# Optimization experiments

Hardware: AMD Instinct MI355X
Metric: run time of the kernel (lower is better)

## Reference

```python
import jax, jax.numpy as jnp
import numpy as np
import math

B, S, H = 2, 2048, 2048
NH, HD = 16, 128
THETA = 10000.0
NEG = -1e9


def make_rope_tables(seq_len, head_dim, theta):
    inv_freq = 1.0 / (theta ** (np.arange(0, head_dim, 2, dtype=np.float32) / head_dim))
    pos = np.arange(seq_len, dtype=np.float32)
    freqs = np.outer(pos, inv_freq)                    # (S, HD/2)
    emb = np.concatenate([freqs, freqs], axis=-1)      # (S, HD)
    return jnp.asarray(np.cos(emb)), jnp.asarray(np.sin(emb))


def setup_inputs() -> dict:
    key = jax.random.key(0)
    k1, k2, k3 = jax.random.split(key, 3)
    hidden_states = jax.random.normal(k1, (B, S, H), dtype=jnp.float32)
    rope_cos, rope_sin = make_rope_tables(S, HD, THETA)
    # additive causal mask [1,1,S,S]
    causal = jnp.tril(jnp.ones((S, S), dtype=bool))
    attention_mask = jnp.where(causal, 0.0, NEG).astype(jnp.float32)[None, None]
    w_qkv = jax.random.normal(k2, (3 * H, H), dtype=jnp.float32) * (1.0 / math.sqrt(H))
    w_o = jax.random.normal(k3, (H, H), dtype=jnp.float32) * (1.0 / math.sqrt(H))
    return {"hidden_states": hidden_states, "rope_cos": rope_cos, "rope_sin": rope_sin,
            "attention_mask": attention_mask, "w_qkv": w_qkv, "w_o": w_o}


def apply_rope(x, cos, sin):
    # x: (B, NH, S, HD); cos/sin: (S, HD)
    half = x.shape[-1] // 2
    x1, x2 = x[..., :half], x[..., half:]
    x_rot = jnp.concatenate([-x2, x1], axis=-1)
    return x * cos[None, None] + x_rot * sin[None, None]


def reference(hidden_states, rope_cos, rope_sin, attention_mask, w_qkv, w_o):
    b, s, h = hidden_states.shape
    qkv = hidden_states @ w_qkv.T                      # (B, S, 3H)
    qkv = qkv.reshape(b, s, 3, NH, HD).transpose(2, 0, 3, 1, 4)  # (3, B, NH, S, HD)
    q, k, v = qkv[0], qkv[1], qkv[2]
    q = apply_rope(q, rope_cos, rope_sin)
    k = apply_rope(k, rope_cos, rope_sin)
    scale = 1.0 / math.sqrt(HD)
    scores = jnp.einsum('bhqd,bhkd->bhqk', q, k) * scale + attention_mask
    probs = jax.nn.softmax(scores.astype(jnp.float32), axis=-1).astype(q.dtype)
    out = jnp.einsum('bhqk,bhkd->bhqd', probs, v)      # (B, NH, S, HD)
    out = out.transpose(0, 2, 1, 3).reshape(b, s, h)
    return out @ w_o.T
```

## Files before the change

kernel.cpp:

```cpp
#include <hip/hip_runtime.h>
#include <stdint.h>

typedef unsigned int u32;
typedef unsigned short u16;

typedef __bf16 bf16x8 __attribute__((ext_vector_type(8)));
typedef float f32x4 __attribute__((ext_vector_type(4)));

struct alignas(16) V16 { u32 a, b, c, d; };

__device__ __forceinline__ u16 f2bf(float x) {
    u32 u = __float_as_uint(x);
    u += 0x7FFFu + ((u >> 16) & 1u);
    return (u16)(u >> 16);
}
__device__ __forceinline__ float bf2f(u16 h) {
    return __uint_as_float(((u32)h) << 16);
}

__device__ __forceinline__ bf16x8 ld_frag(const u16* p) {
    return __builtin_bit_cast(bf16x8, *(const V16*)p);
}

__device__ __forceinline__ void async_cp16(u16* lds_dst, const u16* g_src) {
    __builtin_amdgcn_global_load_lds(
        (__attribute__((address_space(1))) void*)g_src,
        (__attribute__((address_space(3))) void*)lds_dst, 16, 0, 0);
}

__global__ __launch_bounds__(256) void cast_all_kernel(
    const float* __restrict__ hidden, const float* __restrict__ wqkv,
    const float* __restrict__ wo,
    u16* __restrict__ hA, u16* __restrict__ wqb, u16* __restrict__ wob)
{
    int i = blockIdx.x * 256 + threadIdx.x;
    const float* src; u16* dst; int off;
    if (i < 2097152)      { src = hidden; dst = hA;  off = i; }
    else if (i < 5242880) { src = wqkv;   dst = wqb; off = i - 2097152; }
    else                  { src = wo;     dst = wob; off = i - 5242880; }
    const float* p = src + (size_t)off * 4;
    ushort4 o;
    o.x = f2bf(p[0]); o.y = f2bf(p[1]); o.z = f2bf(p[2]); o.w = f2bf(p[3]);
    *(ushort4*)(dst + (size_t)off * 4) = o;
}

__device__ __forceinline__ void stage_half(
    u16* smem, const u16* __restrict__ Ag, const u16* __restrict__ Bg,
    int K, int isB, int kk, int buf, int th, int w, int rg0, int chl)
{
    const u16* G = isB ? Bg : Ag;
    u16* base = smem + isB * 32768 + buf * 16384 + kk * 8192;
    const int kcol = th * 64 + kk * 32;
#pragma unroll
    for (int i = 0; i < 2; ++i) {
        const int s = i * 8 + w;
        const int rg = s * 16 + rg0;
        async_cp16(base + s * 512, G + (size_t)rg * K + kcol + chl * 8);
    }
}

__global__ __launch_bounds__(512, 2) void gemm256(
    const u16* __restrict__ A, const u16* __restrict__ Bt,
    int M, int N, int K, int mode,
    float* __restrict__ Cout,
    u16* __restrict__ Qb, u16* __restrict__ Kb, u16* __restrict__ Vtb)
{
    extern __shared__ u16 smem[];
    const int t = threadIdx.x;
    const int w = t >> 6, l = t & 63;
    const int lr = l & 15, lk = (l >> 4) * 8;
    const int wm16 = (w >> 2) * 8;
    const int wn16 = (w & 3) * 4;
    const int laneoff = lr * 32 + (lk ^ ((lr & 8) ? 16 : 0));
    const int rg0 = l >> 2;
    const int chl = (l & 3) ^ ((l >> 4) & 2);

    const int flat = blockIdx.y * gridDim.x + blockIdx.x;
    const int xcd = flat & 7, slot = flat >> 3;
    const int cpx = gridDim.x >> 3;
    const int ncol = xcd * cpx + slot % cpx;
    const int mrow = slot / cpx;
    const int m0 = mrow * 256, n0 = ncol * 256;

    const u16* Ag = A + (size_t)m0 * K;
    const u16* Bg = Bt + (size_t)n0 * K;

    f32x4 acc[8][4];
#pragma unroll
    for (int i = 0; i < 8; ++i)
#pragma unroll
        for (int j = 0; j < 4; ++j) acc[i][j] = f32x4{0.f, 0.f, 0.f, 0.f};

    const int NT = K >> 6;

    stage_half(smem, Ag, Bg, K, 0, 0, 0, 0, w, rg0, chl);
    stage_half(smem, Ag, Bg, K, 1, 0, 0, 0, w, rg0, chl);
    stage_half(smem, Ag, Bg, K, 0, 1, 0, 0, w, rg0, chl);
    stage_half(smem, Ag, Bg, K, 1, 1, 0, 0, w, rg0, chl);
    stage_half(smem, Ag, Bg, K, 0, 0, 1, 1, w, rg0, chl);
    stage_half(smem, Ag, Bg, K, 1, 0, 1, 1, w, rg0, chl);
    asm volatile("s_waitcnt vmcnt(8)" ::: "memory");
    __builtin_amdgcn_s_barrier();

    for (int tt = 0; tt < NT; tt += 2) {
#pragma unroll
        for (int sub = 0; sub < 2; ++sub) {
            const int tcur = tt + sub;
            const u16* Abuf = smem + sub * 16384;
            const u16* Bbuf = smem + 32768 + sub * 16384;
            bf16x8 bfr[4];
#pragma unroll
            for (int p = 0; p < 4; ++p) {
                const int kk = p >> 1, mh = p & 1;
                const u16* Ab = Abuf + kk * 8192;
                const u16* Bb = Bbuf + kk * 8192;
                if (mh == 0) {
#pragma unroll
                    for (int ni = 0; ni < 4; ++ni)
                        bfr[ni] = ld_frag(Bb + (wn16 + ni) * 512 + laneoff);
                }
                bf16x8 af[4];
#pragma unroll
                for (int i = 0; i < 4; ++i)
                    af[i] = ld_frag(Ab + (wm16 + mh * 4 + i) * 512 + laneoff);

                if (p == 0 && tcur + 1 < NT)
                    stage_half(smem, Ag, Bg, K, 0, 1, sub ^ 1, tcur + 1, w, rg0, chl);
                if (p == 1 && tcur + 1 < NT)
                    stage_half(smem, Ag, Bg, K, 1, 1, sub ^ 1, tcur + 1, w, rg0, chl);
                if (p == 2 && tcur + 2 < NT)
                    stage_half(smem, Ag, Bg, K, 0, 0, sub, tcur + 2, w, rg0, chl);
                if (p == 3 && tcur + 2 < NT)
                    stage_half(smem, Ag, Bg, K, 1, 0, sub, tcur + 2, w, rg0, chl);

                if (p == 1) {
                    if (tcur < NT - 1) asm volatile("s_waitcnt vmcnt(8)" ::: "memory");
                    else               asm volatile("s_waitcnt vmcnt(0)" ::: "memory");
                }
                if (p == 3) {
                    if (tcur < NT - 2)       asm volatile("s_waitcnt vmcnt(8)" ::: "memory");
                    else if (tcur == NT - 2) asm volatile("s_waitcnt vmcnt(4)" ::: "memory");
                }
                __builtin_amdgcn_s_barrier();
                __builtin_amdgcn_s_setprio(1);
#pragma unroll
                for (int i = 0; i < 4; ++i)
#pragma unroll
                    for (int ni = 0; ni < 4; ++ni)
                        acc[mh * 4 + i][ni] = __builtin_amdgcn_mfma_f32_16x16x32_bf16(
                            af[i], bfr[ni], acc[mh * 4 + i][ni], 0, 0, 0);
                __builtin_amdgcn_s_setprio(0);
                __builtin_amdgcn_s_barrier();
            }
        }
    }

    __syncthreads();
    const int lrow4 = (l >> 4) * 4;
    const int wm0 = (w >> 2) * 128, wn0 = (w & 3) * 64;

    if (mode == 1) {
#pragma unroll
        for (int mi = 0; mi < 8; ++mi)
#pragma unroll
            for (int ni = 0; ni < 4; ++ni)
#pragma unroll
                for (int r = 0; r < 4; ++r) {
                    int gr = m0 + wm0 + mi * 16 + lrow4 + r;
                    int gc = n0 + wn0 + ni * 16 + lr;
                    Cout[(size_t)gr * N + gc] = acc[mi][ni][r];
                }
        return;
    }

    const int which = n0 >> 11;
    const int nh0 = (n0 & 2047) >> 7;
    const int bb = m0 >> 11;
    const int s0 = m0 & 2047;

    if (which < 2) {
#pragma unroll
        for (int mi = 0; mi < 8; ++mi)
#pragma unroll
            for (int ni = 0; ni < 4; ++ni)
#pragma unroll
                for (int r = 0; r < 4; ++r)
                    smem[(wm0 + mi * 16 + lrow4 + r) * 256 + wn0 + ni * 16 + lr] =
                        f2bf(acc[mi][ni][r]);
    } else {
#pragma unroll
        for (int mi = 0; mi < 8; ++mi)
#pragma unroll
            for (int ni = 0; ni < 4; ++ni)
#pragma unroll
                for (int r = 0; r < 4; ++r) {
                    int cr = wn0 + ni * 16 + lr;
                    int cc = wm0 + mi * 16 + lrow4 + r;
                    smem[cr * 256 + (cc ^ ((cr & 7) << 3))] = f2bf(acc[mi][ni][r]);
                }
    }
    __syncthreads();

    if (which < 2) {
        u16* dstb = (which == 0 ? Qb : Kb);
#pragma unroll
        for (int ps = 0; ps < 16; ++ps) {
            int chunk = ps * 512 + t;
            int row = chunk >> 5;
            int ce = (chunk & 31) * 8;
            int head = nh0 + (ce >> 7);
            int d = ce & 127;
            *(V16*)&dstb[((size_t)(bb * 16 + head) * 2048 + s0 + row) * 128 + d] =
                *(const V16*)&smem[row * 256 + ce];
        }
    } else {
#pragma unroll
        for (int ps = 0; ps < 16; ++ps) {
            int chunk = ps * 512 + t;
            int drow = chunk >> 5;
            int se = (chunk & 31) * 8;
            int head = nh0 + (drow >> 7);
            int d = drow & 127;
            *(V16*)&Vtb[((size_t)(bb * 16 + head) * 128 + d) * 2048 + s0 + se] =
                *(const V16*)&smem[drow * 256 + (se ^ ((drow & 7) << 3))];
        }
    }
}

__global__ __launch_bounds__(256) void rope_kernel(
    u16* __restrict__ Qb, u16* __restrict__ Kb,
    const float* __restrict__ cosT, const float* __restrict__ sinT, float qscale)
{
    int idx = blockIdx.x * 256 + threadIdx.x;
    int d = (idx & 7) * 8;
    int s = (idx >> 3) & 2047;
    int bh = idx >> 14;
    size_t base = ((size_t)bh * 2048 + s) * 128;
    float c[8], sn[8];
#pragma unroll
    for (int i = 0; i < 8; ++i) {
        c[i]  = cosT[s * 128 + d + i];
        sn[i] = sinT[s * 128 + d + i];
    }
    union U { V16 v; u16 h[8]; };
    U qlo, qhi, klo, khi, a, bq, ak, bk;
    qlo.v = *(const V16*)&Qb[base + d];
    qhi.v = *(const V16*)&Qb[base + d + 64];
    klo.v = *(const V16*)&Kb[base + d];
    khi.v = *(const V16*)&Kb[base + d + 64];
#pragma unroll
    for (int i = 0; i < 8; ++i) {
        float q1 = bf2f(qlo.h[i]), q2 = bf2f(qhi.h[i]);
        a.h[i]  = f2bf((q1 * c[i] - q2 * sn[i]) * qscale);
        bq.h[i] = f2bf((q2 * c[i] + q1 * sn[i]) * qscale);
        float k1 = bf2f(klo.h[i]), k2 = bf2f(khi.h[i]);
        ak.h[i] = f2bf(k1 * c[i] - k2 * sn[i]);
        bk.h[i] = f2bf(k2 * c[i] + k1 * sn[i]);
    }
    *(V16*)&Qb[base + d]      = a.v;
    *(V16*)&Qb[base + d + 64] = bq.v;
    *(V16*)&Kb[base + d]      = ak.v;
    *(V16*)&Kb[base + d + 64] = bk.v;
}

#define PS_LD 72
__global__ __launch_bounds__(256, 2) void flash_attn(
    const u16* __restrict__ Qb, const u16* __restrict__ Kb, const u16* __restrict__ Vtb,
    u16* __restrict__ ctx)
{
    __shared__ u16 Ks[2 * 64 * 128];
    __shared__ u16 Vts[2 * 128 * 64];
    __shared__ u16 Ps[4 * 16 * PS_LD];

    const int t = threadIdx.x, w = t >> 6, l = t & 63;
    const int lr = l & 15, lk = (l >> 4) * 8, lrow4 = (l >> 4) * 4;
    const int hi = l >> 4;
    const int xw = lr & 7;
    const int bh = blockIdx.x;
    const int pidx = blockIdx.y;
    const int wm = w * 16;

    const u16* Qg = Qb + (size_t)bh * 2048 * 128;
    const u16* Kg = Kb + (size_t)bh * 2048 * 128;
    const u16* Vg = Vtb + (size_t)bh * 128 * 2048;
    u16* Pw = &Ps[w * 16 * PS_LD];

    const int krow_l = l >> 4;
    const int vrow_l = l >> 3;
    const int vchk = ((l & 7) ^ vrow_l) * 8;

    const int b = bh >> 4, nh = bh & 15;

#pragma unroll
    for (int half = 0; half < 2; ++half) {
        const int qt = half ? pidx : 31 - pidx;
        const int q0 = qt * 64;

        bf16x8 qfrag[4];
#pragma unroll
        for (int kc = 0; kc < 4; ++kc)
            qfrag[kc] = ld_frag(&Qg[(size_t)(q0 + wm + lr) * 128 + kc * 32 + lk]);

        f32x4 oacc[8];
#pragma unroll
        for (int jo = 0; jo < 8; ++jo) oacc[jo] = f32x4{0.f, 0.f, 0.f, 0.f};
        float l_part[4] = {0.f, 0.f, 0.f, 0.f};

        const int ktiles = qt + 1;

#pragma unroll
        for (int it = 0; it < 4; ++it) {
            const int krow = it * 4 + krow_l;
            const int kchk = ((l & 15) ^ (krow & 7)) * 8;
            async_cp16(&Ks[w * 2048 + it * 512],
                       Kg + (size_t)(w * 16 + krow) * 128 + kchk);
        }
#pragma unroll
        for (int it = 0; it < 4; ++it) {
            const int vrow = w * 32 + it * 8 + vrow_l;
            async_cp16(&Vts[w * 2048 + it * 512],
                       Vg + (size_t)vrow * 2048 + vchk);
        }

        for (int kt = 0; kt < ktiles; ++kt) {
            const int buf = kt & 1;
            if (kt + 1 < ktiles) {
                const int c0n = (kt + 1) * 64;
                const int bo = (buf ^ 1) * 8192;
#pragma unroll
                for (int it = 0; it < 4; ++it) {
                    const int krow = it * 4 + krow_l;
                    const int kchk = ((l & 15) ^ (krow & 7)) * 8;
                    async_cp16(&Ks[bo + w * 2048 + it * 512],
                               Kg + (size_t)(c0n + w * 16 + krow) * 128 + kchk);
                }
#pragma unroll
                for (int it = 0; it < 4; ++it) {
                    const int vrow = w * 32 + it * 8 + vrow_l;
                    async_cp16(&Vts[bo + w * 2048 + it * 512],
                               Vg + (size_t)vrow * 2048 + c0n + vchk);
                }
                asm volatile("s_waitcnt vmcnt(8)" ::: "memory");
            } else {
                asm volatile("s_waitcnt vmcnt(0)" ::: "memory");
            }
            __builtin_amdgcn_s_barrier();

            const u16* Ksb = Ks + buf * 8192;
            const u16* Vsb = Vts + buf * 8192;

            f32x4 pacc[4];
#pragma unroll
            for (int j = 0; j < 4; ++j) pacc[j] = f32x4{0.f, 0.f, 0.f, 0.f};
#pragma unroll
            for (int kc = 0; kc < 4; ++kc) {
                const int kco = ((kc * 4 + hi) ^ xw) * 8;
                bf16x8 bk[4];
#pragma unroll
                for (int j = 0; j < 4; ++j)
                    bk[j] = ld_frag(&Ksb[(j * 16 + lr) * 128 + kco]);
#pragma unroll
                for (int j = 0; j < 4; ++j)
                    pacc[j] = __builtin_amdgcn_mfma_f32_16x16x32_bf16(qfrag[kc], bk[j], pacc[j], 0, 0, 0);
            }

            if (kt == qt) {
#pragma unroll
                for (int j = 0; j < 4; ++j) {
                    const int cl = j * 16 + lr;
#pragma unroll
                    for (int r = 0; r < 4; ++r) {
                        float pv = (cl > wm + lrow4 + r) ? 0.f : __expf(pacc[j][r]);
                        pacc[j][r] = pv;
                        l_part[r] += pv;
                    }
                }
            } else {
#pragma unroll
                for (int j = 0; j < 4; ++j)
#pragma unroll
                    for (int r = 0; r < 4; ++r) {
                        float pv = __expf(pacc[j][r]);
                        pacc[j][r] = pv;
                        l_part[r] += pv;
                    }
            }

#pragma unroll
            for (int j = 0; j < 4; ++j)
#pragma unroll
                for (int r = 0; r < 4; ++r)
                    Pw[(lrow4 + r) * PS_LD + j * 16 + lr] = f2bf(pacc[j][r]);

#pragma unroll
            for (int kc = 0; kc < 2; ++kc) {
                bf16x8 ap = ld_frag(&Pw[lr * PS_LD + kc * 32 + lk]);
                const int vco = ((kc * 4 + hi) ^ xw) * 8;
#pragma unroll
                for (int jo = 0; jo < 8; ++jo) {
                    bf16x8 bv = ld_frag(&Vsb[(jo * 16 + lr) * 64 + vco]);
                    oacc[jo] = __builtin_amdgcn_mfma_f32_16x16x32_bf16(ap, bv, oacc[jo], 0, 0, 0);
                }
            }
            __builtin_amdgcn_s_barrier();
        }

        float linv[4];
#pragma unroll
        for (int r = 0; r < 4; ++r) {
            float s = l_part[r];
#pragma unroll
            for (int dd = 8; dd >= 1; dd >>= 1) s += __shfl_xor(s, dd);
            linv[r] = __builtin_amdgcn_rcpf(s);
        }
#pragma unroll
        for (int jo = 0; jo < 8; ++jo)
#pragma unroll
            for (int r = 0; r < 4; ++r) {
                int srow2 = q0 + wm + lrow4 + r;
                int col = nh * 128 + jo * 16 + lr;
                ctx[((size_t)b * 2048 + srow2) * 2048 + col] = f2bf(oacc[jo][r] * linv[r]);
            }
    }
}

extern "C" void kernel_launch(void* const* d_in, const int* in_sizes, int n_in,
                              void* d_out, int out_size, void* d_ws, size_t ws_size,
                              hipStream_t stream)
{
    (void)in_sizes; (void)n_in; (void)out_size; (void)ws_size;
    const float* hidden = (const float*)d_in[0];
    const float* cosT   = (const float*)d_in[1];
    const float* sinT   = (const float*)d_in[2];
    const float* wqkv   = (const float*)d_in[4];
    const float* wo     = (const float*)d_in[5];
    float* out = (float*)d_out;
    char* ws = (char*)d_ws;

    u16* hA   = (u16*)(ws + 0);
    u16* wqb  = (u16*)(ws + 16777216);
    u16* wob  = (u16*)(ws + 41943040);
    u16* Qb   = (u16*)(ws + 50331648);
    u16* Kb   = (u16*)(ws + 67108864);
    u16* Vtb  = (u16*)(ws + 83886080);
    u16* ctx  = (u16*)(ws + 100663296);

    static bool attr_done = false;
    if (!attr_done) {
        hipFuncSetAttribute((const void*)gemm256,
                            hipFuncAttributeMaxDynamicSharedMemorySize, 131072);
        attr_done = true;
    }

    cast_all_kernel<<<dim3(24576), dim3(256), 0, stream>>>(hidden, wqkv, wo,
                                                           hA, wqb, wob);

    gemm256<<<dim3(24, 16), dim3(512), 131072, stream>>>(hA, wqb, 4096, 6144, 2048, 0,
                                                         nullptr, Qb, Kb, Vtb);
    rope_kernel<<<dim3(2048), dim3(256), 0, stream>>>(Qb, Kb, cosT, sinT,
                                                      0.08838834764831845f);

    flash_attn<<<dim3(32, 16), dim3(256), 0, stream>>>(Qb, Kb, Vtb, ctx);

    gemm256<<<dim3(8, 16), dim3(512), 131072, stream>>>(ctx, wob, 4096, 2048, 2048, 1,
                                                        out, nullptr, nullptr, nullptr);
}
```

Baseline: 387.1 us.

## Replace output GEMM with simpler 128x128 kernel and drop flash-attn double buffering

Adds a new gemm_bt kernel that uses 128x128 tiles, 256 threads and static LDS, and uses it for the output projection in place of the 256-tile gemm256 launch. It also removes double buffering of K/V tiles in flash_attn, so each tile is loaded synchronously between barriers and LDS use per block halves. The smaller LDS footprint may allow more resident blocks, but global-load latency is no longer hidden behind MFMA work. The new GEMM also has no load/compute overlap and uses unswizzled LDS tiles, which may cause bank conflicts.

```diff
diff --git a/kernel.cpp b/kernel.cpp
--- a/kernel.cpp
+++ b/kernel.cpp
@@ -227,6 +227,130 @@
     }
 }
 
+__global__ __launch_bounds__(256) void gemm_bt(
+    const u16* __restrict__ A, const u16* __restrict__ Bt,
+    int M, int N, int K, int mode,
+    float* __restrict__ Cout,
+    u16* __restrict__ Qb, u16* __restrict__ Kb, u16* __restrict__ Vtb)
+{
+    __shared__ u16 smem[17408];
+    u16* As = smem;
+    u16* Bs = smem + 8192;
+
+    const int t = threadIdx.x;
+    const int w = t >> 6, l = t & 63;
+    const int lr = l & 15;
+    const int lk = (l >> 4) * 8;
+
+    const int flat = blockIdx.y * gridDim.x + blockIdx.x;
+    const int xcd = flat & 7, slot = flat >> 3;
+    const int cpx = gridDim.x >> 3;
+    const int ncol = xcd * cpx + slot % cpx;
+    const int mrow = slot / cpx;
+    const int m0 = mrow * 128, n0 = ncol * 128;
+    const int wm = (w >> 1) * 64, wn = (w & 1) * 64;
+
+    f32x4 acc[4][4];
+#pragma unroll
+    for (int i = 0; i < 4; ++i)
+#pragma unroll
+        for (int j = 0; j < 4; ++j) acc[i][j] = f32x4{0.f, 0.f, 0.f, 0.f};
+
+    const u16* Ag = A + (size_t)m0 * K;
+    const u16* Bg = Bt + (size_t)n0 * K;
+    const int srow = l >> 2;
+    const int scol = (l & 3) * 8;
+
+    for (int k0 = 0; k0 < K; k0 += 64) {
+#pragma unroll
+        for (int g = 0; g < 2; ++g) {
+            const int row = w * 32 + g * 16;
+#pragma unroll
+            for (int c = 0; c < 2; ++c) {
+                async_cp16(&As[c * 4096 + row * 32],
+                           Ag + (size_t)(row + srow) * K + k0 + c * 32 + scol);
+                async_cp16(&Bs[c * 4096 + row * 32],
+                           Bg + (size_t)(row + srow) * K + k0 + c * 32 + scol);
+            }
+        }
+        __syncthreads();
+
+#pragma unroll
+        for (int c = 0; c < 2; ++c) {
+            bf16x8 af[4], bf[4];
+#pragma unroll
+            for (int i = 0; i < 4; ++i)
+                af[i] = ld_frag(&As[c * 4096 + (wm + i * 16 + lr) * 32 + lk]);
+#pragma unroll
+            for (int j = 0; j < 4; ++j)
+                bf[j] = ld_frag(&Bs[c * 4096 + (wn + j * 16 + lr) * 32 + lk]);
+#pragma unroll
+            for (int i = 0; i < 4; ++i)
+#pragma unroll
+                for (int j = 0; j < 4; ++j)
+                    acc[i][j] = __builtin_amdgcn_mfma_f32_16x16x32_bf16(af[i], bf[j], acc[i][j], 0, 0, 0);
+        }
+        __syncthreads();
+    }
+
+    const int lrow4 = (l >> 4) * 4;
+    if (mode == 1) {
+#pragma unroll
+        for (int i = 0; i < 4; ++i)
+#pragma unroll
+            for (int j = 0; j < 4; ++j)
+#pragma unroll
+                for (int r = 0; r < 4; ++r) {
+                    int gr = m0 + wm + i * 16 + lrow4 + r;
+                    int gc = n0 + wn + j * 16 + lr;
+                    Cout[(size_t)gr * N + gc] = acc[i][j][r];
+                }
+    } else {
+        const int which = n0 >> 11;
+        const int nh = (n0 & 2047) >> 7;
+        const int bb = m0 >> 11;
+        const int s0 = m0 & 2047;
+        u16* Cs = smem;
+        if (which < 2) {
+#pragma unroll
+            for (int i = 0; i < 4; ++i)
+#pragma unroll
+                for (int j = 0; j < 4; ++j)
+#pragma unroll
+                    for (int r = 0; r < 4; ++r)
+                        Cs[(wm + i * 16 + lrow4 + r) * 136 + wn + j * 16 + lr] =
+                            f2bf(acc[i][j][r]);
+        } else {
+#pragma unroll
+            for (int i = 0; i < 4; ++i)
+#pragma unroll
+                for (int j = 0; j < 4; ++j)
+#pragma unroll
+                    for (int r = 0; r < 4; ++r)
+                        Cs[(wn + j * 16 + lr) * 136 + wm + i * 16 + lrow4 + r] =
+                            f2bf(acc[i][j][r]);
+        }
+        __syncthreads();
+        const int rrow = t >> 4, rcol = (t & 15) * 8;
+        if (which < 2) {
+            u16* dst = (which == 0 ? Qb : Kb) +
+                       ((size_t)(bb * 16 + nh) * 2048 + s0) * 128;
+#pragma unroll
+            for (int it = 0; it < 8; ++it) {
+                int row = it * 16 + rrow;
+                *(V16*)&dst[(size_t)row * 128 + rcol] = *(const V16*)&Cs[row * 136 + rcol];
+            }
+        } else {
+            u16* dst = Vtb + (size_t)(bb * 16 + nh) * 128 * 2048 + s0;
+#pragma unroll
+            for (int it = 0; it < 8; ++it) {
+                int d = it * 16 + rrow;
+                *(V16*)&dst[(size_t)d * 2048 + rcol] = *(const V16*)&Cs[d * 136 + rcol];
+            }
+        }
+    }
+}
+
 __global__ __launch_bounds__(256) void rope_kernel(
     u16* __restrict__ Qb, u16* __restrict__ Kb,
     const float* __restrict__ cosT, const float* __restrict__ sinT, float qscale)
@@ -268,8 +392,8 @@
     const u16* __restrict__ Qb, const u16* __restrict__ Kb, const u16* __restrict__ Vtb,
     u16* __restrict__ ctx)
 {
-    __shared__ u16 Ks[2 * 64 * 128];
-    __shared__ u16 Vts[2 * 128 * 64];
+    __shared__ u16 Ks[64 * 128];
+    __shared__ u16 Vts[128 * 64];
     __shared__ u16 Ps[4 * 16 * PS_LD];
 
     const int t = threadIdx.x, w = t >> 6, l = t & 63;
@@ -307,47 +431,22 @@
         float l_part[4] = {0.f, 0.f, 0.f, 0.f};
 
         const int ktiles = qt + 1;
-
-#pragma unroll
-        for (int it = 0; it < 4; ++it) {
-            const int krow = it * 4 + krow_l;
-            const int kchk = ((l & 15) ^ (krow & 7)) * 8;
-            async_cp16(&Ks[w * 2048 + it * 512],
-                       Kg + (size_t)(w * 16 + krow) * 128 + kchk);
-        }
-#pragma unroll
-        for (int it = 0; it < 4; ++it) {
-            const int vrow = w * 32 + it * 8 + vrow_l;
-            async_cp16(&Vts[w * 2048 + it * 512],
-                       Vg + (size_t)vrow * 2048 + vchk);
-        }
-
         for (int kt = 0; kt < ktiles; ++kt) {
-            const int buf = kt & 1;
-            if (kt + 1 < ktiles) {
-                const int c0n = (kt + 1) * 64;
-                const int bo = (buf ^ 1) * 8192;
-#pragma unroll
-                for (int it = 0; it < 4; ++it) {
-                    const int krow = it * 4 + krow_l;
-                    const int kchk = ((l & 15) ^ (krow & 7)) * 8;
-                    async_cp16(&Ks[bo + w * 2048 + it * 512],
-                               Kg + (size_t)(c0n + w * 16 + krow) * 128 + kchk);
-                }
-#pragma unroll
-                for (int it = 0; it < 4; ++it) {
-                    const int vrow = w * 32 + it * 8 + vrow_l;
-                    async_cp16(&Vts[bo + w * 2048 + it * 512],
-                               Vg + (size_t)vrow * 2048 + c0n + vchk);
-                }
-                asm volatile("s_waitcnt vmcnt(8)" ::: "memory");
-            } else {
-                asm volatile("s_waitcnt vmcnt(0)" ::: "memory");
-            }
-            __builtin_amdgcn_s_barrier();
-
-            const u16* Ksb = Ks + buf * 8192;
-            const u16* Vsb = Vts + buf * 8192;
+            const int c0 = kt * 64;
+#pragma unroll
+            for (int it = 0; it < 4; ++it) {
+                const int krow = it * 4 + krow_l;
+                const int kchk = ((l & 15) ^ (krow & 7)) * 8;
+                async_cp16(&Ks[w * 2048 + it * 512],
+                           Kg + (size_t)(c0 + w * 16 + krow) * 128 + kchk);
+            }
+#pragma unroll
+            for (int it = 0; it < 4; ++it) {
+                const int vrow = w * 32 + it * 8 + vrow_l;
+                async_cp16(&Vts[w * 2048 + it * 512],
+                           Vg + (size_t)vrow * 2048 + c0 + vchk);
+            }
+            __syncthreads();
 
             f32x4 pacc[4];
 #pragma unroll
@@ -358,7 +457,7 @@
                 bf16x8 bk[4];
 #pragma unroll
                 for (int j = 0; j < 4; ++j)
-                    bk[j] = ld_frag(&Ksb[(j * 16 + lr) * 128 + kco]);
+                    bk[j] = ld_frag(&Ks[(j * 16 + lr) * 128 + kco]);
 #pragma unroll
                 for (int j = 0; j < 4; ++j)
                     pacc[j] = __builtin_amdgcn_mfma_f32_16x16x32_bf16(qfrag[kc], bk[j], pacc[j], 0, 0, 0);
@@ -398,11 +497,11 @@
                 const int vco = ((kc * 4 + hi) ^ xw) * 8;
 #pragma unroll
                 for (int jo = 0; jo < 8; ++jo) {
-                    bf16x8 bv = ld_frag(&Vsb[(jo * 16 + lr) * 64 + vco]);
+                    bf16x8 bv = ld_frag(&Vts[(jo * 16 + lr) * 64 + vco]);
                     oacc[jo] = __builtin_amdgcn_mfma_f32_16x16x32_bf16(ap, bv, oacc[jo], 0, 0, 0);
                 }
             }
-            __builtin_amdgcn_s_barrier();
+            __syncthreads();
         }
 
         float linv[4];
@@ -462,6 +561,6 @@
 
     flash_attn<<<dim3(32, 16), dim3(256), 0, stream>>>(Qb, Kb, Vtb, ctx);
 
-    gemm256<<<dim3(8, 16), dim3(512), 131072, stream>>>(ctx, wob, 4096, 2048, 2048, 1,
-                                                        out, nullptr, nullptr, nullptr);
-}
+    gemm_bt<<<dim3(16, 32), dim3(256), 0, stream>>>(ctx, wob, 4096, 2048, 2048, 1,
+                                                    out, nullptr, nullptr, nullptr);
+}
```

After: 377.4 us. -2.5%, faster.
